# Performance work log

Measured on AMD Instinct MI355X. Metric: run time of the kernel, lower is better.

Reference implementation:

```python
import jax, jax.numpy as jnp
import numpy as np

B, C, H, W = 8, 128, 64, 64
INTER = C // 2

def setup_inputs() -> dict:
    key = jax.random.key(0)
    ks = jax.random.split(key, 9)
    s = 0.05
    return {
        "x": jax.random.normal(ks[0], (B, C, H, W), dtype=jnp.float32),
        "theta_w": jax.random.normal(ks[1], (INTER, C), dtype=jnp.float32) * s,
        "theta_b": jax.random.normal(ks[2], (INTER,), dtype=jnp.float32) * s,
        "phi_w": jax.random.normal(ks[3], (INTER, C), dtype=jnp.float32) * s,
        "phi_b": jax.random.normal(ks[4], (INTER,), dtype=jnp.float32) * s,
        "g_w": jax.random.normal(ks[5], (INTER, C), dtype=jnp.float32) * s,
        "g_b": jax.random.normal(ks[6], (INTER,), dtype=jnp.float32) * s,
        "out_w": jax.random.normal(ks[7], (C, INTER), dtype=jnp.float32) * s,
        "out_b": jax.random.normal(ks[8], (C,), dtype=jnp.float32) * s,
    }

def reference(x, theta_w, theta_b, phi_w, phi_b, g_w, g_b, out_w, out_b):
    b, c, h, w = x.shape
    xf = x.reshape(b, c, h * w)                                   # [b, C, n]
    # 1x1 convs == per-pixel channel matmuls
    theta = jnp.einsum('oc,bcn->bno', theta_w, xf) + theta_b       # [b, n, inter]
    phi = jnp.einsum('oc,bcn->bon', phi_w, xf) + phi_b[:, None]    # [b, inter, n]
    g = jnp.einsum('oc,bcn->bno', g_w, xf) + g_b                   # [b, n, inter]
    attn = jax.nn.softmax(jnp.einsum('bno,bom->bnm', theta, phi), axis=-1)  # [b, n, n]
    y = jnp.einsum('bnm,bmo->bon', attn, g)                        # [b, inter, n]
    out = jnp.einsum('oc,bcn->bon', out_w, y) + out_b[:, None]     # [b, C, n]
    return out.reshape(b, c, h, w) + x
```

## Files before the change

kernel.cpp:

```cpp
#include <hip/hip_runtime.h>
#include <hip/hip_bf16.h>
#include <cstdint>
#include <cmath>

#define N_PIX 4096
#define CH    128
#define DD    64
#define NBATCH 8
#define NT    32

typedef unsigned short u16;
typedef __attribute__((ext_vector_type(8))) short bf8_t;
typedef __attribute__((ext_vector_type(4))) float f4_t;
typedef __attribute__((ext_vector_type(16))) float f16v;
typedef uint32_t u32x4 __attribute__((ext_vector_type(4)));
typedef uint32_t u32x2 __attribute__((ext_vector_type(2)));

#define L2E 1.44269504088896340736f

#if __has_builtin(__builtin_amdgcn_exp2f)
  #define EXP2(x) __builtin_amdgcn_exp2f(x)
#else
  #define EXP2(x) exp2f(x)
#endif

__device__ __forceinline__ u16 f2b(float f) {
  return __builtin_bit_cast(u16, __float2bfloat16(f));
}
__device__ __forceinline__ float b2f(u16 h) {
  union { uint32_t u; float f; } v; v.u = ((uint32_t)h) << 16;
  return v.f;
}
__device__ __forceinline__ uint32_t pack2(float a, float b) {
  return (uint32_t)f2b(a) | ((uint32_t)f2b(b) << 16);
}
__device__ __forceinline__ float max3f(float a, float b, float c) {
  return fmaxf(fmaxf(a, b), c);
}
__device__ __forceinline__ f4_t mfma16(bf8_t a, bf8_t b, f4_t c) {
  return __builtin_amdgcn_mfma_f32_16x16x32_bf16(a, b, c, 0, 0, 0);
}
__device__ __forceinline__ f16v mfma32(bf8_t a, bf8_t b, f16v c) {
  return __builtin_amdgcn_mfma_f32_32x32x16_bf16(a, b, c, 0, 0, 0);
}
__device__ __forceinline__ void pl32swap(uint32_t &a, uint32_t &b) {
  u32x2 r = __builtin_amdgcn_permlane32_swap(a, b, false, false);
  a = r[0];
  b = r[1];
}

__global__ __launch_bounds__(256) void proj_kernel(
    const float* __restrict__ x,
    const float* __restrict__ tw, const float* __restrict__ tb,
    const float* __restrict__ pw, const float* __restrict__ pb,
    const float* __restrict__ gw, const float* __restrict__ gb,
    u16* __restrict__ theta_h, u16* __restrict__ phi_h, u16* __restrict__ gt_h) {
  __shared__ __align__(16) u16 smem[12800];
  const int blk = blockIdx.x;
  const int b  = blk >> 6;
  const int n0 = (blk & 63) << 6;
  const int tid = threadIdx.x;

  #pragma unroll
  for (int i = 0; i < 8; ++i) {
    int idx = tid + i * 256;
    int px = (idx & 15) * 4;
    int c  = idx >> 4;
    int m  = px >> 2;
    float4 v = *(const float4*)(x + ((size_t)b * CH + c) * N_PIX + n0 + px);
    int base = px * 136 + ((((c >> 3) ^ m) & 15) << 3) + (c & 7);
    smem[base]       = f2b(v.x);
    smem[base + 136] = f2b(v.y);
    smem[base + 272] = f2b(v.z);
    smem[base + 408] = f2b(v.w);
  }
  __syncthreads();

  const int lane = tid & 63;
  const int w    = tid >> 6;
  const int l4   = lane >> 4, l15 = lane & 15;

  bf8_t bw[3][4];
  float bias[3];
  #pragma unroll
  for (int nt = 0; nt < 3; ++nt) {
    int op = 16 * (3 * w + nt) + l15;
    const float* wrow; float bv; float scl;
    if (op < 64)       { wrow = tw + op * CH;          bv = tb[op];        scl = L2E; }
    else if (op < 128) { wrow = pw + (op - 64) * CH;   bv = pb[op - 64];   scl = 1.f; }
    else               { wrow = gw + (op - 128) * CH;  bv = gb[op - 128];  scl = 1.f; }
    bias[nt] = bv * scl;
    #pragma unroll
    for (int ks = 0; ks < 4; ++ks) {
      const float* p = wrow + 32 * ks + l4 * 8;
      bf8_t v;
      #pragma unroll
      for (int j = 0; j < 8; ++j) v[j] = (short)f2b(p[j] * scl);
      bw[nt][ks] = v;
    }
  }

  f4_t acc[4][3];
  #pragma unroll
  for (int mt = 0; mt < 4; ++mt)
    #pragma unroll
    for (int nt = 0; nt < 3; ++nt) acc[mt][nt] = (f4_t){0.f, 0.f, 0.f, 0.f};

  #pragma unroll
  for (int mt = 0; mt < 4; ++mt) {
    int row = l15 + 16 * mt;
    #pragma unroll
    for (int ks = 0; ks < 4; ++ks) {
      int ch = ((4 * ks + l4) ^ (row >> 2)) & 15;
      bf8_t a = *(const bf8_t*)&smem[row * 136 + (ch << 3)];
      #pragma unroll
      for (int nt = 0; nt < 3; ++nt)
        acc[mt][nt] = mfma16(a, bw[nt][ks], acc[mt][nt]);
    }
  }
  __syncthreads();

  #pragma unroll
  for (int nt = 0; nt < 3; ++nt) {
    int op = 16 * (3 * w + nt) + l15;
    #pragma unroll
    for (int mt = 0; mt < 4; ++mt) {
      #pragma unroll
      for (int r = 0; r < 4; ++r) {
        int ql = 16 * mt + l4 * 4 + r;
        smem[ql * 200 + op] = f2b(acc[mt][nt][r] + bias[nt]);
      }
    }
  }
  __syncthreads();

  #pragma unroll
  for (int i = 0; i < 4; ++i) {
    int idx = tid + i * 256;
    int q  = idx >> 4;
    int ch = idx & 15;
    uint4 v = *(const uint4*)&smem[q * 200 + ch * 8];
    if (ch < 8)
      *(uint4*)(theta_h + ((size_t)b * N_PIX + n0 + q) * DD + ch * 8) = v;
    else
      *(uint4*)(phi_h + ((size_t)b * N_PIX + n0 + q) * DD + (ch - 8) * 8) = v;
  }
  #pragma unroll
  for (int i = 0; i < 2; ++i) {
    int idx = tid + i * 256;
    int o = idx >> 3;
    int j = idx & 7;
    uint4 v;
    uint32_t* vp = (uint32_t*)&v;
    #pragma unroll
    for (int k = 0; k < 4; ++k) {
      u16 lo = smem[(8 * j + 2 * k) * 200 + 128 + o];
      u16 hi = smem[(8 * j + 2 * k + 1) * 200 + 128 + o];
      vp[k] = (uint32_t)lo | ((uint32_t)hi << 16);
    }
    *(uint4*)(gt_h + ((size_t)b * DD + o) * N_PIX + n0 + 8 * j) = v;
  }
}

__global__ __launch_bounds__(512, 4) void attn_kernel(
    const u16* __restrict__ theta_h, const u16* __restrict__ phi_h,
    const u16* __restrict__ gt_h,
    const float* __restrict__ ow, const float* __restrict__ ob,
    const float* __restrict__ x, float* __restrict__ out) {
  __shared__ __align__(16) u16 smem[32768];

  const int bid = blockIdx.x;
  const int lb  = (bid & 7) * 64 + (bid >> 3);
  const int b   = lb >> 6;
  const int q0  = (lb & 63) << 6;
  const int tid = threadIdx.x;
  const int l   = tid & 63;
  const int w   = tid >> 6;
  const int qg  = w & 1;
  const int mh  = w >> 1;
  const int l31 = l & 31;
  const int hi  = l >> 5;

  bf8_t th[4];
  {
    const u16* trow = theta_h + ((size_t)b * N_PIX + q0 + 32 * qg + l31) * DD;
    #pragma unroll
    for (int kk = 0; kk < 4; ++kk)
      th[kk] = *(const bf8_t*)(trow + 16 * kk + 8 * hi);
  }

  const bf8_t onesA = __builtin_bit_cast(bf8_t,
      (u32x4){0x3F803F80u, 0x3F803F80u, 0x3F803F80u, 0x3F803F80u});

  f16v yacc[2];
  #pragma unroll
  for (int ot = 0; ot < 2; ++ot)
    #pragma unroll
    for (int r = 0; r < 16; ++r) yacc[ot][r] = 0.f;
  f16v y2;
  #pragma unroll
  for (int r = 0; r < 16; ++r) y2[r] = 0.f;
  float m_ = -1e30f;

  const int pr  = tid >> 3, pc = tid & 7;
  const int go  = tid >> 4, gc = tid & 15;
  const u16* phA = phi_h + ((size_t)b * N_PIX + pr) * DD + pc * 8;
  const u16* gtA = gt_h + ((size_t)b * DD + go) * N_PIX + gc * 8;
  const int pO0 = pr * 64 + ((pc ^ (pr & 7)) << 3);
  const int pO1 = pO0 + 4096;
  const int gO0 = 8192 + go * 128 + ((gc ^ (go & 7)) << 3);
  const int gO1 = gO0 + 4096;

  uint4 v0, v1, v2, v3;
  #define LOADS(kb_) do {                                              \
    v0 = *(const uint4*)(phA + (size_t)(kb_) * 8192);                  \
    v1 = *(const uint4*)(phA + (size_t)(kb_) * 8192 + 4096);           \
    v2 = *(const uint4*)(gtA + (size_t)(kb_) * 128);                   \
    v3 = *(const uint4*)(gtA + (size_t)(kb_) * 128 + 32 * (size_t)N_PIX); \
  } while (0)
  #define WRITES(buf_) do {                                            \
    u16* base_ = smem + (buf_) * 16384;                                \
    *(uint4*)(base_ + pO0) = v0;                                       \
    *(uint4*)(base_ + pO1) = v1;                                       \
    *(uint4*)(base_ + gO0) = v2;                                       \
    *(uint4*)(base_ + gO1) = v3;                                       \
  } while (0)

  LOADS(0); WRITES(0);
  __syncthreads();

  const int prow  = 32 * mh + l31;
  const int pbase = prow * 64;
  const int pkey  = prow & 7;

  #pragma unroll 2
  for (int t = 0; t < NT; ++t) {
    const int cur = t & 1;
    if (t < NT - 1) LOADS(t + 1);
    const u16* pb = smem + cur * 16384;
    const u16* gb = pb + 8192;

    f16v st;
    #pragma unroll
    for (int r = 0; r < 16; ++r) st[r] = 0.f;
    __builtin_amdgcn_s_setprio(1);
    #pragma unroll
    for (int kk = 0; kk < 4; ++kk) {
      bf8_t a = *(const bf8_t*)(pb + pbase + (((2 * kk + hi) ^ pkey) << 3));
      st = mfma32(a, th[kk], st);
    }
    __builtin_amdgcn_s_setprio(0);

    float t0 = max3f(st[0],  st[1],  st[2]);
    float t1 = max3f(st[3],  st[4],  st[5]);
    float t2 = max3f(st[6],  st[7],  st[8]);
    float t3 = max3f(st[9],  st[10], st[11]);
    float t4 = max3f(st[12], st[13], st[14]);
    float pmax = fmaxf(max3f(t0, t1, t2), max3f(t3, t4, st[15]));
    pmax = fmaxf(pmax, __shfl_xor(pmax, 32));

    if (!__all(pmax <= m_ + 8.f)) {
      float mn = fmaxf(m_, pmax);
      float sc = EXP2(m_ - mn);
      m_ = mn;
      y2[0] *= sc;
      #pragma unroll
      for (int ot = 0; ot < 2; ++ot)
        #pragma unroll
        for (int r = 0; r < 16; ++r) yacc[ot][r] *= sc;
    }

    #pragma unroll
    for (int r = 0; r < 16; ++r) st[r] = EXP2(st[r] - m_);

    uint32_t c0 = pack2(st[0],  st[1]),  c1 = pack2(st[2],  st[3]);
    uint32_t c2 = pack2(st[4],  st[5]),  c3 = pack2(st[6],  st[7]);
    uint32_t c4 = pack2(st[8],  st[9]),  c5 = pack2(st[10], st[11]);
    uint32_t c6 = pack2(st[12], st[13]), c7 = pack2(st[14], st[15]);
    pl32swap(c0, c2); pl32swap(c1, c3);
    pl32swap(c4, c6); pl32swap(c5, c7);
    bf8_t pf0 = __builtin_bit_cast(bf8_t, (u32x4){c0, c1, c2, c3});
    bf8_t pf1 = __builtin_bit_cast(bf8_t, (u32x4){c4, c5, c6, c7});

    __builtin_amdgcn_s_setprio(1);
    y2 = mfma32(onesA, pf0, y2);
    y2 = mfma32(onesA, pf1, y2);
    #pragma unroll
    for (int ot = 0; ot < 2; ++ot) {
      int orow  = 32 * ot + l31;
      int obase = orow * 128;
      int okey  = orow & 7;
      bf8_t g0 = *(const bf8_t*)(gb + obase + ((((mh << 2) + hi)     ^ okey) << 3));
      yacc[ot] = mfma32(g0, pf0, yacc[ot]);
      bf8_t g1 = *(const bf8_t*)(gb + obase + ((((mh << 2) + 2 + hi) ^ okey) << 3));
      yacc[ot] = mfma32(g1, pf1, yacc[ot]);
    }
    __builtin_amdgcn_s_setprio(0);

    if (t < NT - 1) WRITES(cur ^ 1);
    __syncthreads();
  }
  #undef LOADS
  #undef WRITES

  float l_ = y2[0];

  #pragma unroll
  for (int ot = 0; ot < 2; ++ot)
    #pragma unroll
    for (int r = 0; r < 16; ++r) {
      int o = 32 * ot + (r & 3) + 8 * (r >> 2) + 4 * hi;
      smem[(((qg * 4 + mh) * 64 + o) << 5) + l31] = f2b(yacc[ot][r]);
    }
  float* ml = (float*)(smem + 16384);
  if (hi == 0) {
    ml[(qg * 4 + mh) * 64 + l31]      = m_;
    ml[(qg * 4 + mh) * 64 + 32 + l31] = l_;
  }
  __syncthreads();

  u16* y_lds = smem + 17408;
  {
    const int qg2 = tid >> 8;
    const int rem = tid & 255;
    const int qq  = rem & 31;
    const int og  = rem >> 5;
    float mi[4], li[4];
    #pragma unroll
    for (int i = 0; i < 4; ++i) {
      mi[i] = ml[(qg2 * 4 + i) * 64 + qq];
      li[i] = ml[(qg2 * 4 + i) * 64 + 32 + qq];
    }
    float M = fmaxf(fmaxf(mi[0], mi[1]), fmaxf(mi[2], mi[3]));
    float e[4], L = 0.f;
    #pragma unroll
    for (int i = 0; i < 4; ++i) { e[i] = EXP2(mi[i] - M); L += li[i] * e[i]; }
    float invL = 1.0f / L;
    float acc[8];
    #pragma unroll
    for (int oo = 0; oo < 8; ++oo) {
      int o = og * 8 + oo;
      float a = 0.f;
      #pragma unroll
      for (int i = 0; i < 4; ++i)
        a += b2f(smem[(((qg2 * 4 + i) * 64 + o) << 5) + qq]) * e[i];
      acc[oo] = a * invL;
    }
    uint4 ov;
    ov.x = pack2(acc[0], acc[1]);
    ov.y = pack2(acc[2], acc[3]);
    ov.z = pack2(acc[4], acc[5]);
    ov.w = pack2(acc[6], acc[7]);
    *(uint4*)(y_lds + (32 * qg2 + qq) * 72 + og * 8) = ov;
  }
  __syncthreads();

  {
    const int ct = w & 3;
    const int qt = w >> 2;
    f16v oacc;
    #pragma unroll
    for (int r = 0; r < 16; ++r) oacc[r] = 0.f;
    #pragma unroll
    for (int kk = 0; kk < 4; ++kk) {
      const float* wp = ow + (size_t)(32 * ct + l31) * DD + 16 * kk + 8 * hi;
      bf8_t av;
      #pragma unroll
      for (int j = 0; j < 8; ++j) av[j] = (short)f2b(wp[j]);
      bf8_t bv = *(const bf8_t*)(y_lds + (32 * qt + l31) * 72 + 16 * kk + 8 * hi);
      oacc = mfma32(av, bv, oacc);
    }
    #pragma unroll
    for (int r = 0; r < 16; ++r) {
      int c = 32 * ct + (r & 3) + 8 * (r >> 2) + 4 * hi;
      size_t gi = ((size_t)b * CH + c) * N_PIX + q0 + 32 * qt + l31;
      out[gi] = oacc[r] + ob[c] + x[gi];
    }
  }
}

extern "C" void kernel_launch(void* const* d_in, const int* in_sizes, int n_in,
                              void* d_out, int out_size, void* d_ws, size_t ws_size,
                              hipStream_t stream) {
  const float* x  = (const float*)d_in[0];
  const float* tw = (const float*)d_in[1];
  const float* tb = (const float*)d_in[2];
  const float* pw = (const float*)d_in[3];
  const float* pb = (const float*)d_in[4];
  const float* gw = (const float*)d_in[5];
  const float* gb = (const float*)d_in[6];
  const float* ow = (const float*)d_in[7];
  const float* ob = (const float*)d_in[8];
  float* out = (float*)d_out;

  const size_t sz = (size_t)NBATCH * N_PIX * DD;
  u16* theta_h = (u16*)d_ws;
  u16* phi_h   = theta_h + sz;
  u16* gt_h    = phi_h + sz;

  proj_kernel<<<512, 256, 0, stream>>>(x, tw, tb, pw, pb, gw, gb,
                                       theta_h, phi_h, gt_h);
  attn_kernel<<<512, 512, 0, stream>>>(theta_h, phi_h, gt_h, ow, ob, x, out);
}
```

Measured before the change: 78.46 us.

## Process two query tiles per block to reuse phi/g tiles, row sums via VALU

Each attention block now handles 128 queries (two 64-query sub-tiles A and B) instead of 64, so every phi and g tile staged in LDS feeds twice the MFMA work and the grid halves to 256 blocks. The row-sum accumulation moves from a ones-matrix MFMA to VALU adds plus a cross-half shuffle. The epilogue runs twice in sequence, once per sub-tile. This roughly doubles accumulator register use (launch bounds lowered to 2 blocks per CU), and 256 blocks may underfill the CUs on this device.

```diff
diff --git a/kernel.cpp b/kernel.cpp
--- a/kernel.cpp
+++ b/kernel.cpp
@@ -162,7 +162,7 @@
   }
 }
 
-__global__ __launch_bounds__(512, 4) void attn_kernel(
+__global__ __launch_bounds__(512, 2) void attn_kernel(
     const u16* __restrict__ theta_h, const u16* __restrict__ phi_h,
     const u16* __restrict__ gt_h,
     const float* __restrict__ ow, const float* __restrict__ ob,
@@ -170,9 +170,9 @@
   __shared__ __align__(16) u16 smem[32768];
 
   const int bid = blockIdx.x;
-  const int lb  = (bid & 7) * 64 + (bid >> 3);
-  const int b   = lb >> 6;
-  const int q0  = (lb & 63) << 6;
+  const int lb  = (bid & 7) * 32 + (bid >> 3);
+  const int b   = lb >> 5;
+  const int q0  = (lb & 31) << 7;
   const int tid = threadIdx.x;
   const int l   = tid & 63;
   const int w   = tid >> 6;
@@ -181,26 +181,24 @@
   const int l31 = l & 31;
   const int hi  = l >> 5;
 
-  bf8_t th[4];
+  bf8_t thA[4], thB[4];
   {
-    const u16* trow = theta_h + ((size_t)b * N_PIX + q0 + 32 * qg + l31) * DD;
-    #pragma unroll
-    for (int kk = 0; kk < 4; ++kk)
-      th[kk] = *(const bf8_t*)(trow + 16 * kk + 8 * hi);
-  }
-
-  const bf8_t onesA = __builtin_bit_cast(bf8_t,
-      (u32x4){0x3F803F80u, 0x3F803F80u, 0x3F803F80u, 0x3F803F80u});
-
-  f16v yacc[2];
+    const u16* trowA = theta_h + ((size_t)b * N_PIX + q0 + 32 * qg + l31) * DD;
+    const u16* trowB = trowA + 64 * DD;
+    #pragma unroll
+    for (int kk = 0; kk < 4; ++kk) {
+      thA[kk] = *(const bf8_t*)(trowA + 16 * kk + 8 * hi);
+      thB[kk] = *(const bf8_t*)(trowB + 16 * kk + 8 * hi);
+    }
+  }
+
+  f16v yaccA[2], yaccB[2];
   #pragma unroll
   for (int ot = 0; ot < 2; ++ot)
     #pragma unroll
-    for (int r = 0; r < 16; ++r) yacc[ot][r] = 0.f;
-  f16v y2;
-  #pragma unroll
-  for (int r = 0; r < 16; ++r) y2[r] = 0.f;
-  float m_ = -1e30f;
+    for (int r = 0; r < 16; ++r) { yaccA[ot][r] = 0.f; yaccB[ot][r] = 0.f; }
+  float mA = -1e30f, lA = 0.f;
+  float mB = -1e30f, lB = 0.f;
 
   const int pr  = tid >> 3, pc = tid & 7;
   const int go  = tid >> 4, gc = tid & 15;
@@ -233,67 +231,106 @@
   const int pbase = prow * 64;
   const int pkey  = prow & 7;
 
-  #pragma unroll 2
   for (int t = 0; t < NT; ++t) {
     const int cur = t & 1;
     if (t < NT - 1) LOADS(t + 1);
     const u16* pb = smem + cur * 16384;
     const u16* gb = pb + 8192;
 
-    f16v st;
-    #pragma unroll
-    for (int r = 0; r < 16; ++r) st[r] = 0.f;
+    f16v stA, stB;
+    #pragma unroll
+    for (int r = 0; r < 16; ++r) { stA[r] = 0.f; stB[r] = 0.f; }
     __builtin_amdgcn_s_setprio(1);
     #pragma unroll
     for (int kk = 0; kk < 4; ++kk) {
       bf8_t a = *(const bf8_t*)(pb + pbase + (((2 * kk + hi) ^ pkey) << 3));
-      st = mfma32(a, th[kk], st);
+      stA = mfma32(a, thA[kk], stA);
+      stB = mfma32(a, thB[kk], stB);
     }
     __builtin_amdgcn_s_setprio(0);
 
-    float t0 = max3f(st[0],  st[1],  st[2]);
-    float t1 = max3f(st[3],  st[4],  st[5]);
-    float t2 = max3f(st[6],  st[7],  st[8]);
-    float t3 = max3f(st[9],  st[10], st[11]);
-    float t4 = max3f(st[12], st[13], st[14]);
-    float pmax = fmaxf(max3f(t0, t1, t2), max3f(t3, t4, st[15]));
-    pmax = fmaxf(pmax, __shfl_xor(pmax, 32));
-
-    if (!__all(pmax <= m_ + 8.f)) {
-      float mn = fmaxf(m_, pmax);
-      float sc = EXP2(m_ - mn);
-      m_ = mn;
-      y2[0] *= sc;
-      #pragma unroll
-      for (int ot = 0; ot < 2; ++ot)
+    {
+      float t0 = max3f(stA[0],  stA[1],  stA[2]);
+      float t1 = max3f(stA[3],  stA[4],  stA[5]);
+      float t2 = max3f(stA[6],  stA[7],  stA[8]);
+      float t3 = max3f(stA[9],  stA[10], stA[11]);
+      float t4 = max3f(stA[12], stA[13], stA[14]);
+      float pmax = fmaxf(max3f(t0, t1, t2), max3f(t3, t4, stA[15]));
+      pmax = fmaxf(pmax, __shfl_xor(pmax, 32));
+      if (!__all(pmax <= mA + 8.f)) {
+        float mn = fmaxf(mA, pmax);
+        float sc = EXP2(mA - mn);
+        mA = mn;
+        lA *= sc;
         #pragma unroll
-        for (int r = 0; r < 16; ++r) yacc[ot][r] *= sc;
-    }
-
-    #pragma unroll
-    for (int r = 0; r < 16; ++r) st[r] = EXP2(st[r] - m_);
-
-    uint32_t c0 = pack2(st[0],  st[1]),  c1 = pack2(st[2],  st[3]);
-    uint32_t c2 = pack2(st[4],  st[5]),  c3 = pack2(st[6],  st[7]);
-    uint32_t c4 = pack2(st[8],  st[9]),  c5 = pack2(st[10], st[11]);
-    uint32_t c6 = pack2(st[12], st[13]), c7 = pack2(st[14], st[15]);
-    pl32swap(c0, c2); pl32swap(c1, c3);
-    pl32swap(c4, c6); pl32swap(c5, c7);
-    bf8_t pf0 = __builtin_bit_cast(bf8_t, (u32x4){c0, c1, c2, c3});
-    bf8_t pf1 = __builtin_bit_cast(bf8_t, (u32x4){c4, c5, c6, c7});
+        for (int ot = 0; ot < 2; ++ot)
+          #pragma unroll
+          for (int r = 0; r < 16; ++r) yaccA[ot][r] *= sc;
+      }
+      #pragma unroll
+      for (int r = 0; r < 16; ++r) stA[r] = EXP2(stA[r] - mA);
+      float s0 = stA[0] + stA[1],   s1 = stA[2] + stA[3];
+      float s2 = stA[4] + stA[5],   s3 = stA[6] + stA[7];
+      float s4 = stA[8] + stA[9],   s5 = stA[10] + stA[11];
+      float s6 = stA[12] + stA[13], s7 = stA[14] + stA[15];
+      lA += ((s0 + s1) + (s2 + s3)) + ((s4 + s5) + (s6 + s7));
+    }
+    uint32_t a0 = pack2(stA[0],  stA[1]),  a1 = pack2(stA[2],  stA[3]);
+    uint32_t a2 = pack2(stA[4],  stA[5]),  a3 = pack2(stA[6],  stA[7]);
+    uint32_t a4 = pack2(stA[8],  stA[9]),  a5 = pack2(stA[10], stA[11]);
+    uint32_t a6 = pack2(stA[12], stA[13]), a7 = pack2(stA[14], stA[15]);
+    pl32swap(a0, a2); pl32swap(a1, a3);
+    pl32swap(a4, a6); pl32swap(a5, a7);
+    bf8_t pfA0 = __builtin_bit_cast(bf8_t, (u32x4){a0, a1, a2, a3});
+    bf8_t pfA1 = __builtin_bit_cast(bf8_t, (u32x4){a4, a5, a6, a7});
+
+    {
+      float t0 = max3f(stB[0],  stB[1],  stB[2]);
+      float t1 = max3f(stB[3],  stB[4],  stB[5]);
+      float t2 = max3f(stB[6],  stB[7],  stB[8]);
+      float t3 = max3f(stB[9],  stB[10], stB[11]);
+      float t4 = max3f(stB[12], stB[13], stB[14]);
+      float pmax = fmaxf(max3f(t0, t1, t2), max3f(t3, t4, stB[15]));
+      pmax = fmaxf(pmax, __shfl_xor(pmax, 32));
+      if (!__all(pmax <= mB + 8.f)) {
+        float mn = fmaxf(mB, pmax);
+        float sc = EXP2(mB - mn);
+        mB = mn;
+        lB *= sc;
+        #pragma unroll
+        for (int ot = 0; ot < 2; ++ot)
+          #pragma unroll
+          for (int r = 0; r < 16; ++r) yaccB[ot][r] *= sc;
+      }
+      #pragma unroll
+      for (int r = 0; r < 16; ++r) stB[r] = EXP2(stB[r] - mB);
+      float s0 = stB[0] + stB[1],   s1 = stB[2] + stB[3];
+      float s2 = stB[4] + stB[5],   s3 = stB[6] + stB[7];
+      float s4 = stB[8] + stB[9],   s5 = stB[10] + stB[11];
+      float s6 = stB[12] + stB[13], s7 = stB[14] + stB[15];
+      lB += ((s0 + s1) + (s2 + s3)) + ((s4 + s5) + (s6 + s7));
+    }
+    uint32_t b0 = pack2(stB[0],  stB[1]),  b1 = pack2(stB[2],  stB[3]);
+    uint32_t b2 = pack2(stB[4],  stB[5]),  b3 = pack2(stB[6],  stB[7]);
+    uint32_t b4 = pack2(stB[8],  stB[9]),  b5 = pack2(stB[10], stB[11]);
+    uint32_t b6 = pack2(stB[12], stB[13]), b7 = pack2(stB[14], stB[15]);
+    pl32swap(b0, b2); pl32swap(b1, b3);
+    pl32swap(b4, b6); pl32swap(b5, b7);
+    bf8_t pfB0 = __builtin_bit_cast(bf8_t, (u32x4){b0, b1, b2, b3});
+    bf8_t pfB1 = __builtin_bit_cast(bf8_t, (u32x4){b4, b5, b6, b7});
 
     __builtin_amdgcn_s_setprio(1);
-    y2 = mfma32(onesA, pf0, y2);
-    y2 = mfma32(onesA, pf1, y2);
     #pragma unroll
     for (int ot = 0; ot < 2; ++ot) {
       int orow  = 32 * ot + l31;
       int obase = orow * 128;
       int okey  = orow & 7;
       bf8_t g0 = *(const bf8_t*)(gb + obase + ((((mh << 2) + hi)     ^ okey) << 3));
-      yacc[ot] = mfma32(g0, pf0, yacc[ot]);
+      yaccA[ot] = mfma32(g0, pfA0, yaccA[ot]);
+      yaccB[ot] = mfma32(g0, pfB0, yaccB[ot]);
       bf8_t g1 = *(const bf8_t*)(gb + obase + ((((mh << 2) + 2 + hi) ^ okey) << 3));
-      yacc[ot] = mfma32(g1, pf1, yacc[ot]);
+      yaccA[ot] = mfma32(g1, pfA1, yaccA[ot]);
+      yaccB[ot] = mfma32(g1, pfB1, yaccB[ot]);
     }
     __builtin_amdgcn_s_setprio(0);
 
@@ -303,23 +340,24 @@
   #undef LOADS
   #undef WRITES
 
-  float l_ = y2[0];
+  lA += __shfl_xor(lA, 32);
+  lB += __shfl_xor(lB, 32);
+
+  float* ml = (float*)(smem + 16384);
+  u16* y_lds = smem + 17408;
 
   #pragma unroll
   for (int ot = 0; ot < 2; ++ot)
     #pragma unroll
     for (int r = 0; r < 16; ++r) {
       int o = 32 * ot + (r & 3) + 8 * (r >> 2) + 4 * hi;
-      smem[(((qg * 4 + mh) * 64 + o) << 5) + l31] = f2b(yacc[ot][r]);
-    }
-  float* ml = (float*)(smem + 16384);
+      smem[(((qg * 4 + mh) * 64 + o) << 5) + l31] = f2b(yaccA[ot][r]);
+    }
   if (hi == 0) {
-    ml[(qg * 4 + mh) * 64 + l31]      = m_;
-    ml[(qg * 4 + mh) * 64 + 32 + l31] = l_;
-  }
-  __syncthreads();
-
-  u16* y_lds = smem + 17408;
+    ml[(qg * 4 + mh) * 64 + l31]      = mA;
+    ml[(qg * 4 + mh) * 64 + 32 + l31] = lA;
+  }
+  __syncthreads();
   {
     const int qg2 = tid >> 8;
     const int rem = tid & 255;
@@ -354,7 +392,6 @@
     *(uint4*)(y_lds + (32 * qg2 + qq) * 72 + og * 8) = ov;
   }
   __syncthreads();
-
   {
     const int ct = w & 3;
     const int qt = w >> 2;
@@ -374,6 +411,76 @@
     for (int r = 0; r < 16; ++r) {
       int c = 32 * ct + (r & 3) + 8 * (r >> 2) + 4 * hi;
       size_t gi = ((size_t)b * CH + c) * N_PIX + q0 + 32 * qt + l31;
+      out[gi] = oacc[r] + ob[c] + x[gi];
+    }
+  }
+  __syncthreads();
+
+  #pragma unroll
+  for (int ot = 0; ot < 2; ++ot)
+    #pragma unroll
+    for (int r = 0; r < 16; ++r) {
+      int o = 32 * ot + (r & 3) + 8 * (r >> 2) + 4 * hi;
+      smem[(((qg * 4 + mh) * 64 + o) << 5) + l31] = f2b(yaccB[ot][r]);
+    }
+  if (hi == 0) {
+    ml[(qg * 4 + mh) * 64 + l31]      = mB;
+    ml[(qg * 4 + mh) * 64 + 32 + l31] = lB;
+  }
+  __syncthreads();
+  {
+    const int qg2 = tid >> 8;
+    const int rem = tid & 255;
+    const int qq  = rem & 31;
+    const int og  = rem >> 5;
+    float mi[4], li[4];
+    #pragma unroll
+    for (int i = 0; i < 4; ++i) {
+      mi[i] = ml[(qg2 * 4 + i) * 64 + qq];
+      li[i] = ml[(qg2 * 4 + i) * 64 + 32 + qq];
+    }
+    float M = fmaxf(fmaxf(mi[0], mi[1]), fmaxf(mi[2], mi[3]));
+    float e[4], L = 0.f;
+    #pragma unroll
+    for (int i = 0; i < 4; ++i) { e[i] = EXP2(mi[i] - M); L += li[i] * e[i]; }
+    float invL = 1.0f / L;
+    float acc[8];
+    #pragma unroll
+    for (int oo = 0; oo < 8; ++oo) {
+      int o = og * 8 + oo;
+      float a = 0.f;
+      #pragma unroll
+      for (int i = 0; i < 4; ++i)
+        a += b2f(smem[(((qg2 * 4 + i) * 64 + o) << 5) + qq]) * e[i];
+      acc[oo] = a * invL;
+    }
+    uint4 ov;
+    ov.x = pack2(acc[0], acc[1]);
+    ov.y = pack2(acc[2], acc[3]);
+    ov.z = pack2(acc[4], acc[5]);
+    ov.w = pack2(acc[6], acc[7]);
+    *(uint4*)(y_lds + (32 * qg2 + qq) * 72 + og * 8) = ov;
+  }
+  __syncthreads();
+  {
+    const int ct = w & 3;
+    const int qt = w >> 2;
+    f16v oacc;
+    #pragma unroll
+    for (int r = 0; r < 16; ++r) oacc[r] = 0.f;
+    #pragma unroll
+    for (int kk = 0; kk < 4; ++kk) {
+      const float* wp = ow + (size_t)(32 * ct + l31) * DD + 16 * kk + 8 * hi;
+      bf8_t av;
+      #pragma unroll
+      for (int j = 0; j < 8; ++j) av[j] = (short)f2b(wp[j]);
+      bf8_t bv = *(const bf8_t*)(y_lds + (32 * qt + l31) * 72 + 16 * kk + 8 * hi);
+      oacc = mfma32(av, bv, oacc);
+    }
+    #pragma unroll
+    for (int r = 0; r < 16; ++r) {
+      int c = 32 * ct + (r & 3) + 8 * (r >> 2) + 4 * hi;
+      size_t gi = ((size_t)b * CH + c) * N_PIX + q0 + 64 + 32 * qt + l31;
       out[gi] = oacc[r] + ob[c] + x[gi];
     }
   }
@@ -400,5 +507,5 @@
 
   proj_kernel<<<512, 256, 0, stream>>>(x, tw, tb, pw, pb, gw, gb,
                                        theta_h, phi_h, gt_h);
-  attn_kernel<<<512, 512, 0, stream>>>(theta_h, phi_h, gt_h, ow, ob, x, out);
-}
+  attn_kernel<<<256, 512, 0, stream>>>(theta_h, phi_h, gt_h, ow, ob, x, out);
+}
```

Measured after the change: 77.62 us (median of 2 runs). About the same (-1.1%).

## Share K/V tiles across two query groups with 1024-thread attention blocks

Applied to the files above, without the earlier changes.

Doubles the attention block to 1024 threads covering 128 queries, so each phi/g tile loaded into shared memory serves twice as many queries. Each thread now issues half as many global loads per tile, and the grid shrinks to 256 blocks. The epilogue is serialized over the two query halves, reusing the same shared buffers with extra barriers. The cost is fewer blocks (256 on a large-CU device), possibly lower occupancy under launch_bounds(1024,4), and a longer serialized epilogue.

```diff
diff --git a/kernel.cpp b/kernel.cpp
--- a/kernel.cpp
+++ b/kernel.cpp
@@ -162,7 +162,7 @@
   }
 }
 
-__global__ __launch_bounds__(512, 4) void attn_kernel(
+__global__ __launch_bounds__(1024, 4) void attn_kernel(
     const u16* __restrict__ theta_h, const u16* __restrict__ phi_h,
     const u16* __restrict__ gt_h,
     const float* __restrict__ ow, const float* __restrict__ ob,
@@ -170,20 +170,23 @@
   __shared__ __align__(16) u16 smem[32768];
 
   const int bid = blockIdx.x;
-  const int lb  = (bid & 7) * 64 + (bid >> 3);
-  const int b   = lb >> 6;
-  const int q0  = (lb & 63) << 6;
+  const int lb  = (bid & 7) * 32 + (bid >> 3);
+  const int b   = lb >> 5;
+  const int q0  = (lb & 31) << 7;
   const int tid = threadIdx.x;
   const int l   = tid & 63;
   const int w   = tid >> 6;
-  const int qg  = w & 1;
-  const int mh  = w >> 1;
+  const int qs  = w >> 3;
+  const int wq  = w & 7;
+  const int qg  = wq & 1;
+  const int mh  = wq >> 1;
   const int l31 = l & 31;
   const int hi  = l >> 5;
 
   bf8_t th[4];
   {
-    const u16* trow = theta_h + ((size_t)b * N_PIX + q0 + 32 * qg + l31) * DD;
+    const u16* trow =
+        theta_h + ((size_t)b * N_PIX + q0 + 64 * qs + 32 * qg + l31) * DD;
     #pragma unroll
     for (int kk = 0; kk < 4; ++kk)
       th[kk] = *(const bf8_t*)(trow + 16 * kk + 8 * hi);
@@ -207,23 +210,17 @@
   const u16* phA = phi_h + ((size_t)b * N_PIX + pr) * DD + pc * 8;
   const u16* gtA = gt_h + ((size_t)b * DD + go) * N_PIX + gc * 8;
   const int pO0 = pr * 64 + ((pc ^ (pr & 7)) << 3);
-  const int pO1 = pO0 + 4096;
   const int gO0 = 8192 + go * 128 + ((gc ^ (go & 7)) << 3);
-  const int gO1 = gO0 + 4096;
-
-  uint4 v0, v1, v2, v3;
+
+  uint4 v0, v1;
   #define LOADS(kb_) do {                                              \
     v0 = *(const uint4*)(phA + (size_t)(kb_) * 8192);                  \
-    v1 = *(const uint4*)(phA + (size_t)(kb_) * 8192 + 4096);           \
-    v2 = *(const uint4*)(gtA + (size_t)(kb_) * 128);                   \
-    v3 = *(const uint4*)(gtA + (size_t)(kb_) * 128 + 32 * (size_t)N_PIX); \
+    v1 = *(const uint4*)(gtA + (size_t)(kb_) * 128);                   \
   } while (0)
   #define WRITES(buf_) do {                                            \
     u16* base_ = smem + (buf_) * 16384;                                \
     *(uint4*)(base_ + pO0) = v0;                                       \
-    *(uint4*)(base_ + pO1) = v1;                                       \
-    *(uint4*)(base_ + gO0) = v2;                                       \
-    *(uint4*)(base_ + gO1) = v3;                                       \
+    *(uint4*)(base_ + gO0) = v1;                                       \
   } while (0)
 
   LOADS(0); WRITES(0);
@@ -305,77 +302,84 @@
 
   float l_ = y2[0];
 
-  #pragma unroll
-  for (int ot = 0; ot < 2; ++ot)
-    #pragma unroll
-    for (int r = 0; r < 16; ++r) {
-      int o = 32 * ot + (r & 3) + 8 * (r >> 2) + 4 * hi;
-      smem[(((qg * 4 + mh) * 64 + o) << 5) + l31] = f2b(yacc[ot][r]);
-    }
   float* ml = (float*)(smem + 16384);
-  if (hi == 0) {
-    ml[(qg * 4 + mh) * 64 + l31]      = m_;
-    ml[(qg * 4 + mh) * 64 + 32 + l31] = l_;
-  }
-  __syncthreads();
-
   u16* y_lds = smem + 17408;
-  {
-    const int qg2 = tid >> 8;
-    const int rem = tid & 255;
-    const int qq  = rem & 31;
-    const int og  = rem >> 5;
-    float mi[4], li[4];
-    #pragma unroll
-    for (int i = 0; i < 4; ++i) {
-      mi[i] = ml[(qg2 * 4 + i) * 64 + qq];
-      li[i] = ml[(qg2 * 4 + i) * 64 + 32 + qq];
-    }
-    float M = fmaxf(fmaxf(mi[0], mi[1]), fmaxf(mi[2], mi[3]));
-    float e[4], L = 0.f;
-    #pragma unroll
-    for (int i = 0; i < 4; ++i) { e[i] = EXP2(mi[i] - M); L += li[i] * e[i]; }
-    float invL = 1.0f / L;
-    float acc[8];
-    #pragma unroll
-    for (int oo = 0; oo < 8; ++oo) {
-      int o = og * 8 + oo;
-      float a = 0.f;
-      #pragma unroll
-      for (int i = 0; i < 4; ++i)
-        a += b2f(smem[(((qg2 * 4 + i) * 64 + o) << 5) + qq]) * e[i];
-      acc[oo] = a * invL;
-    }
-    uint4 ov;
-    ov.x = pack2(acc[0], acc[1]);
-    ov.y = pack2(acc[2], acc[3]);
-    ov.z = pack2(acc[4], acc[5]);
-    ov.w = pack2(acc[6], acc[7]);
-    *(uint4*)(y_lds + (32 * qg2 + qq) * 72 + og * 8) = ov;
-  }
-  __syncthreads();
-
-  {
-    const int ct = w & 3;
-    const int qt = w >> 2;
-    f16v oacc;
-    #pragma unroll
-    for (int r = 0; r < 16; ++r) oacc[r] = 0.f;
-    #pragma unroll
-    for (int kk = 0; kk < 4; ++kk) {
-      const float* wp = ow + (size_t)(32 * ct + l31) * DD + 16 * kk + 8 * hi;
-      bf8_t av;
-      #pragma unroll
-      for (int j = 0; j < 8; ++j) av[j] = (short)f2b(wp[j]);
-      bf8_t bv = *(const bf8_t*)(y_lds + (32 * qt + l31) * 72 + 16 * kk + 8 * hi);
-      oacc = mfma32(av, bv, oacc);
-    }
-    #pragma unroll
-    for (int r = 0; r < 16; ++r) {
-      int c = 32 * ct + (r & 3) + 8 * (r >> 2) + 4 * hi;
-      size_t gi = ((size_t)b * CH + c) * N_PIX + q0 + 32 * qt + l31;
-      out[gi] = oacc[r] + ob[c] + x[gi];
-    }
+
+  #pragma unroll
+  for (int s = 0; s < 2; ++s) {
+    if (qs == s) {
+      #pragma unroll
+      for (int ot = 0; ot < 2; ++ot)
+        #pragma unroll
+        for (int r = 0; r < 16; ++r) {
+          int o = 32 * ot + (r & 3) + 8 * (r >> 2) + 4 * hi;
+          smem[(((qg * 4 + mh) * 64 + o) << 5) + l31] = f2b(yacc[ot][r]);
+        }
+      if (hi == 0) {
+        ml[(qg * 4 + mh) * 64 + l31]      = m_;
+        ml[(qg * 4 + mh) * 64 + 32 + l31] = l_;
+      }
+    }
+    __syncthreads();
+
+    if (tid < 512) {
+      const int qg2 = tid >> 8;
+      const int rem = tid & 255;
+      const int qq  = rem & 31;
+      const int og  = rem >> 5;
+      float mi[4], li[4];
+      #pragma unroll
+      for (int i = 0; i < 4; ++i) {
+        mi[i] = ml[(qg2 * 4 + i) * 64 + qq];
+        li[i] = ml[(qg2 * 4 + i) * 64 + 32 + qq];
+      }
+      float M = fmaxf(fmaxf(mi[0], mi[1]), fmaxf(mi[2], mi[3]));
+      float e[4], L = 0.f;
+      #pragma unroll
+      for (int i = 0; i < 4; ++i) { e[i] = EXP2(mi[i] - M); L += li[i] * e[i]; }
+      float invL = 1.0f / L;
+      float acc[8];
+      #pragma unroll
+      for (int oo = 0; oo < 8; ++oo) {
+        int o = og * 8 + oo;
+        float a = 0.f;
+        #pragma unroll
+        for (int i = 0; i < 4; ++i)
+          a += b2f(smem[(((qg2 * 4 + i) * 64 + o) << 5) + qq]) * e[i];
+        acc[oo] = a * invL;
+      }
+      uint4 ov;
+      ov.x = pack2(acc[0], acc[1]);
+      ov.y = pack2(acc[2], acc[3]);
+      ov.z = pack2(acc[4], acc[5]);
+      ov.w = pack2(acc[6], acc[7]);
+      *(uint4*)(y_lds + (32 * qg2 + qq) * 72 + og * 8) = ov;
+    }
+    __syncthreads();
+
+    if (w < 8) {
+      const int ct = w & 3;
+      const int qt = w >> 2;
+      f16v oacc;
+      #pragma unroll
+      for (int r = 0; r < 16; ++r) oacc[r] = 0.f;
+      #pragma unroll
+      for (int kk = 0; kk < 4; ++kk) {
+        const float* wp = ow + (size_t)(32 * ct + l31) * DD + 16 * kk + 8 * hi;
+        bf8_t av;
+        #pragma unroll
+        for (int j = 0; j < 8; ++j) av[j] = (short)f2b(wp[j]);
+        bf8_t bv = *(const bf8_t*)(y_lds + (32 * qt + l31) * 72 + 16 * kk + 8 * hi);
+        oacc = mfma32(av, bv, oacc);
+      }
+      #pragma unroll
+      for (int r = 0; r < 16; ++r) {
+        int c = 32 * ct + (r & 3) + 8 * (r >> 2) + 4 * hi;
+        size_t gi = ((size_t)b * CH + c) * N_PIX + q0 + 64 * s + 32 * qt + l31;
+        out[gi] = oacc[r] + ob[c] + x[gi];
+      }
+    }
+    __syncthreads();
   }
 }
 
@@ -400,5 +404,5 @@
 
   proj_kernel<<<512, 256, 0, stream>>>(x, tw, tb, pw, pb, gw, gb,
                                        theta_h, phi_h, gt_h);
-  attn_kernel<<<512, 512, 0, stream>>>(theta_h, phi_h, gt_h, ow, ob, x, out);
-}
+  attn_kernel<<<256, 1024, 0, stream>>>(theta_h, phi_h, gt_h, ow, ob, x, out);
+}
```

After: 79.16 us. No clear change (+0.9%).
